# Optimization experiments

Measured on AMD Instinct MI355X. Metric: run time of the kernel, lower is better.

Reference implementation:

```python
import jax, jax.numpy as jnp
import numpy as np

E = 256
H = 512
LN_EPS = 1e-5
NORM_EPS = 1e-12


def setup_inputs() -> dict:
    key = jax.random.key(0)
    ks = jax.random.split(key, 8)
    B, N, M = 8, 128, 128
    track_features = jax.random.normal(ks[0], (B, N, E), dtype=jnp.float32)
    det_features = jax.random.normal(ks[1], (B, M, E), dtype=jnp.float32)
    # MLP params (torch Linear default init style: uniform, but values irrelevant for correctness harness)
    lim1 = 1.0 / np.sqrt(3 * E)
    W1 = jax.random.uniform(ks[2], (3 * E, H), minval=-lim1, maxval=lim1, dtype=jnp.float32)
    b1 = jax.random.uniform(ks[3], (H,), minval=-lim1, maxval=lim1, dtype=jnp.float32)
    gamma = jnp.ones((H,), dtype=jnp.float32)
    beta = jnp.zeros((H,), dtype=jnp.float32)
    lim2 = 1.0 / np.sqrt(H)
    W2 = jax.random.uniform(ks[4], (H, 1), minval=-lim2, maxval=lim2, dtype=jnp.float32)
    b2 = jax.random.uniform(ks[5], (1,), minval=-lim2, maxval=lim2, dtype=jnp.float32)
    return {"track_features": track_features, "det_features": det_features,
            "W1": W1, "b1": b1, "gamma": gamma, "beta": beta, "W2": W2, "b2": b2}


def _l2_normalize(x):
    # F.normalize(x, dim=-1): x / max(||x||_2, eps)
    n = jnp.sqrt(jnp.sum(x * x, axis=-1, keepdims=True))
    return x / jnp.maximum(n, NORM_EPS)


def reference(track_features, det_features, W1, b1, gamma, beta, W2, b2):
    t = _l2_normalize(track_features)   # (B, N, E)
    d = _l2_normalize(det_features)     # (B, M, E)
    tb = t[:, :, None, :]               # (B, N, 1, E)
    db = d[:, None, :, :]               # (B, 1, M, E)
    B, N, _ = t.shape
    M = d.shape[1]
    diff = jnp.abs(tb - db)                                  # (B, N, M, E)
    pair = jnp.concatenate([jnp.broadcast_to(tb, (B, N, M, E)),
                            jnp.broadcast_to(db, (B, N, M, E)),
                            diff], axis=-1)                  # (B, N, M, 3E)
    h = jnp.einsum('bnme,eh->bnmh', pair, W1) + b1           # (B, N, M, H)
    mu = jnp.mean(h, axis=-1, keepdims=True)
    var = jnp.mean((h - mu) ** 2, axis=-1, keepdims=True)
    h = (h - mu) * jax.lax.rsqrt(var + LN_EPS) * gamma + beta
    h = h * jax.nn.sigmoid(h)                                # SiLU
    out = jnp.einsum('bnmh,ho->bnmo', h, W2)[..., 0] + b2[0]  # (B, N, M)
    return out
```

## Files before the change

kernel.cpp:

```cpp
#include <hip/hip_runtime.h>
#include <hip/hip_bf16.h>
#include <cstdint>

typedef __bf16 bf16x8 __attribute__((ext_vector_type(8)));
typedef float f32x4 __attribute__((ext_vector_type(4)));

#define E_DIM 256
#define H_DIM 512
#define TSTR 260

__global__ __launch_bounds__(256)
void w1conv_kernel(const float* __restrict__ W1, __bf16* __restrict__ W1cc) {
    int u = blockIdx.x * 256 + threadIdx.x;
    int j   = u & 3;
    int h   = (u >> 2) & 511;
    int c   = (u >> 11) & 7;
    int mat = u >> 14;
    bf16x8 v;
#pragma unroll
    for (int i = 0; i < 8; ++i)
        v[i] = (__bf16)W1[(size_t)(mat * 256 + c * 32 + j * 8 + i) * H_DIM + h];
    *(bf16x8*)(W1cc + ((size_t)(mat * 8 + c) * 512 + h) * 32 + j * 8) = v;
}

__global__ __launch_bounds__(512, 4)
void pq_mfma_kernel(const float* __restrict__ track, const float* __restrict__ det,
                    const __bf16* __restrict__ W1cc, const float* __restrict__ b1,
                    float* __restrict__ P, float* __restrict__ Q) {
    __shared__ __align__(16) __bf16 Ash[32 * 256];
    __shared__ float sclS[32];

    int tid  = threadIdx.x;
    int lane = tid & 63;
    int wave = tid >> 6;
    int lq   = lane >> 4;
    int lc   = lane & 15;

    int blk  = blockIdx.x;
    int mat  = blk >> 6;
    int rowg = (blk >> 1) & 31;
    int half = blk & 1;
    int r0   = rowg * 32;
    int h0   = half * 256;
    const float* src = mat ? det : track;

#pragma unroll
    for (int i = 0; i < 4; ++i) {
        int row = wave * 4 + i;
        float4 x = ((const float4*)(src + (size_t)(r0 + row) * E_DIM))[lane];
        float ss = x.x*x.x + x.y*x.y + x.z*x.z + x.w*x.w;
#pragma unroll
        for (int off = 32; off > 0; off >>= 1) ss += __shfl_xor(ss, off);
        if (lane == 0) sclS[row] = 1.0f / fmaxf(sqrtf(ss), 1e-12f);
    }
    __syncthreads();

#pragma unroll
    for (int r = 0; r < 2; ++r) {
        int row = r * 16 + lc;
        float st = sclS[row];
        const float* gp = src + (size_t)(r0 + row) * E_DIM + wave * 32 + lq * 8;
        float4 t0 = *(const float4*)gp;
        float4 t1 = *(const float4*)(gp + 4);
        bf16x8 v;
        v[0] = (__bf16)(t0.x * st); v[1] = (__bf16)(t0.y * st);
        v[2] = (__bf16)(t0.z * st); v[3] = (__bf16)(t0.w * st);
        v[4] = (__bf16)(t1.x * st); v[5] = (__bf16)(t1.y * st);
        v[6] = (__bf16)(t1.z * st); v[7] = (__bf16)(t1.w * st);
        *(bf16x8*)&Ash[(size_t)(r * 512 + wave * 64 + lane) * 8] = v;
    }
    __syncthreads();

    const uint4* Wg = (const uint4*)W1cc + (mat ? 16384 : 0);
    int hb = h0 + wave * 32 + lc;
    bf16x8 bwA[2], bwB[2];
#pragma unroll
    for (int ht = 0; ht < 2; ++ht)
        bwA[ht] = __builtin_bit_cast(bf16x8, Wg[(hb + ht * 16) * 4 + lq]);

    f32x4 acc[2][2];
#pragma unroll
    for (int pt = 0; pt < 2; ++pt)
#pragma unroll
        for (int ht = 0; ht < 2; ++ht)
            acc[pt][ht] = (f32x4){0.f, 0.f, 0.f, 0.f};

#pragma unroll
    for (int c = 0; c < 8; ++c) {
        bf16x8* cur = (c & 1) ? bwB : bwA;
        bf16x8* nxt = (c & 1) ? bwA : bwB;
        if (c < 7) {
#pragma unroll
            for (int ht = 0; ht < 2; ++ht)
                nxt[ht] = __builtin_bit_cast(bf16x8, Wg[(c + 1) * 2048 + (hb + ht * 16) * 4 + lq]);
        }
#pragma unroll
        for (int pt = 0; pt < 2; ++pt) {
            bf16x8 af = *(const bf16x8*)&Ash[(size_t)((pt * 8 + c) * 64 + lane) * 8];
#pragma unroll
            for (int ht = 0; ht < 2; ++ht)
                acc[pt][ht] = __builtin_amdgcn_mfma_f32_16x16x32_bf16(cur[ht], af, acc[pt][ht], 0, 0, 0);
        }
    }

    float* dst = mat ? Q : P;
#pragma unroll
    for (int ht = 0; ht < 2; ++ht) {
        int h = h0 + wave * 32 + ht * 16 + lq * 4;
        f32x4 bvv = (f32x4){0.f, 0.f, 0.f, 0.f};
        if (!mat) bvv = *(const f32x4*)&b1[h];
#pragma unroll
        for (int pt = 0; pt < 2; ++pt) {
            f32x4 o = acc[pt][ht] + bvv;
            *(f32x4*)&dst[(size_t)(r0 + pt * 16 + lc) * H_DIM + h] = o;
        }
    }
}

__global__ __launch_bounds__(512, 4)
void main_kernel(const float* __restrict__ track, const float* __restrict__ det,
                 const __bf16* __restrict__ W1cc,
                 const float* __restrict__ P, const float* __restrict__ Q,
                 const float* __restrict__ gamma, const float* __restrict__ beta,
                 const float* __restrict__ W2, const float* __restrict__ b2,
                 float* __restrict__ out) {
    __shared__ __align__(16) char SMEM[49408];
    __bf16* Ash  = (__bf16*)SMEM;
    float*  tsl  = (float*)(SMEM + 32768);
    float*  dsl  = (float*)(SMEM + 41088);
    float*  LNr1 = (float*)(SMEM + 32768);
    float*  LNr2 = (float*)(SMEM + 35072);
    float*  Red2 = (float*)(SMEM + 37376);
    float*  MuS  = (float*)(SMEM + 39680);
    float*  RsS  = (float*)(SMEM + 39936);
    __shared__ float sclT[8], sclD[8];

    int tid  = threadIdx.x;
    int lane = tid & 63;
    int wave = tid >> 6;
    int lq   = lane >> 4;
    int lc   = lane & 15;

    int blk = blockIdx.x;
    int b   = blk >> 8;
    int n0  = ((blk >> 4) & 15) * 8;
    int m0  = (blk & 15) * 8;

    float4 tstage = ((const float4*)(track + (size_t)(b * 128 + n0 + wave) * E_DIM))[lane];
    float4 dstage = ((const float4*)(det   + (size_t)(b * 128 + m0 + wave) * E_DIM))[lane];

    const uint4* Wg = (const uint4*)W1cc + 32768;
    int hb = wave * 64 + lc;
    bf16x8 bwA[4], bwB[4];
#pragma unroll
    for (int ht = 0; ht < 4; ++ht)
        bwA[ht] = __builtin_bit_cast(bf16x8, Wg[(hb + ht * 16) * 4 + lq]);

    {
        float a = tstage.x*tstage.x + tstage.y*tstage.y + tstage.z*tstage.z + tstage.w*tstage.w;
        float d = dstage.x*dstage.x + dstage.y*dstage.y + dstage.z*dstage.z + dstage.w*dstage.w;
#pragma unroll
        for (int off = 32; off > 0; off >>= 1) { a += __shfl_xor(a, off); d += __shfl_xor(d, off); }
        if (lane == 0) {
            sclT[wave] = 1.0f / fmaxf(sqrtf(a), 1e-12f);
            sclD[wave] = 1.0f / fmaxf(sqrtf(d), 1e-12f);
        }
    }
    *(float4*)&tsl[wave * TSTR + lane * 4] = tstage;
    *(float4*)&dsl[wave * TSTR + lane * 4] = dstage;
    __syncthreads();

    {
        int k0 = wave * 32 + lq * 8;
        int ml = lane & 7;
        float sd = sclD[ml];
        const float* dr = dsl + ml * TSTR + k0;
        float4 d0 = *(const float4*)dr;
        float4 d1 = *(const float4*)(dr + 4);
#pragma unroll
        for (int r = 0; r < 4; ++r) {
            int nl = r * 2 + (lc >> 3);
            float st = sclT[nl];
            const float* tr = tsl + nl * TSTR + k0;
            float4 t0 = *(const float4*)tr;
            float4 t1 = *(const float4*)(tr + 4);
            bf16x8 v;
            v[0] = (__bf16)fabsf(t0.x * st - d0.x * sd);
            v[1] = (__bf16)fabsf(t0.y * st - d0.y * sd);
            v[2] = (__bf16)fabsf(t0.z * st - d0.z * sd);
            v[3] = (__bf16)fabsf(t0.w * st - d0.w * sd);
            v[4] = (__bf16)fabsf(t1.x * st - d1.x * sd);
            v[5] = (__bf16)fabsf(t1.y * st - d1.y * sd);
            v[6] = (__bf16)fabsf(t1.z * st - d1.z * sd);
            v[7] = (__bf16)fabsf(t1.w * st - d1.w * sd);
            *(bf16x8*)&Ash[(size_t)(r * 512 + wave * 64 + lane) * 8] = v;
        }
    }

    const float* Pb = P + (size_t)(b * 128 + n0) * H_DIM;
    const float* Qb = Q + (size_t)(b * 128 + m0) * H_DIM;
    f32x4 acc[4][4];
    {
        f32x4 qv[4];
#pragma unroll
        for (int ht = 0; ht < 4; ++ht)
            qv[ht] = *(const f32x4*)&Qb[(size_t)(lc & 7) * H_DIM + wave * 64 + ht * 16 + lq * 4];
#pragma unroll
        for (int pt = 0; pt < 4; ++pt) {
            int n = pt * 2 + (lc >> 3);
#pragma unroll
            for (int ht = 0; ht < 4; ++ht) {
                f32x4 pv = *(const f32x4*)&Pb[(size_t)n * H_DIM + wave * 64 + ht * 16 + lq * 4];
                acc[pt][ht] = pv + qv[ht];
            }
        }
    }
    __syncthreads();

#pragma unroll
    for (int c = 0; c < 8; ++c) {
        bf16x8* cur = (c & 1) ? bwB : bwA;
        bf16x8* nxt = (c & 1) ? bwA : bwB;
        if (c < 7) {
#pragma unroll
            for (int ht = 0; ht < 4; ++ht)
                nxt[ht] = __builtin_bit_cast(bf16x8, Wg[(c + 1) * 2048 + (hb + ht * 16) * 4 + lq]);
        }
#pragma unroll
        for (int pt = 0; pt < 4; ++pt) {
            bf16x8 af = *(const bf16x8*)&Ash[(size_t)((pt * 8 + c) * 64 + lane) * 8];
#pragma unroll
            for (int ht = 0; ht < 4; ++ht)
                acc[pt][ht] = __builtin_amdgcn_mfma_f32_16x16x32_bf16(cur[ht], af, acc[pt][ht], 0, 0, 0);
        }
    }

#pragma unroll
    for (int pt = 0; pt < 4; ++pt) {
        float s1 = 0.f, s2 = 0.f;
#pragma unroll
        for (int ht = 0; ht < 4; ++ht)
#pragma unroll
            for (int rg = 0; rg < 4; ++rg) {
                float v = acc[pt][ht][rg];
                s1 += v; s2 += v * v;
            }
        s1 += __shfl_xor(s1, 16); s2 += __shfl_xor(s2, 16);
        s1 += __shfl_xor(s1, 32); s2 += __shfl_xor(s2, 32);
        if (lq == 0) {
            LNr1[(pt * 16 + lc) * 9 + wave] = s1;
            LNr2[(pt * 16 + lc) * 9 + wave] = s2;
        }
    }
    __syncthreads();
    if (tid < 64) {
        float S1 = 0.f, S2 = 0.f;
#pragma unroll
        for (int w = 0; w < 8; ++w) { S1 += LNr1[tid * 9 + w]; S2 += LNr2[tid * 9 + w]; }
        float mu = S1 * (1.0f / 512.0f);
        float var = S2 * (1.0f / 512.0f) - mu * mu;
        MuS[tid] = mu;
        RsS[tid] = rsqrtf(var + 1e-5f);
    }
    __syncthreads();

    float mus[4], rss[4];
#pragma unroll
    for (int pt = 0; pt < 4; ++pt) { mus[pt] = MuS[pt * 16 + lc]; rss[pt] = RsS[pt * 16 + lc]; }
    float ca[4] = {0.f, 0.f, 0.f, 0.f};
#pragma unroll
    for (int ht = 0; ht < 4; ++ht) {
        int h = wave * 64 + ht * 16 + lq * 4;
        f32x4 g  = *(const f32x4*)&gamma[h];
        f32x4 bb = *(const f32x4*)&beta[h];
        f32x4 w  = *(const f32x4*)&W2[h];
#pragma unroll
        for (int pt = 0; pt < 4; ++pt) {
#pragma unroll
            for (int rg = 0; rg < 4; ++rg) {
                float x = (acc[pt][ht][rg] - mus[pt]) * rss[pt] * g[rg] + bb[rg];
                float sg = __builtin_amdgcn_rcpf(1.0f + __expf(-x));
                ca[pt] += x * sg * w[rg];
            }
        }
    }
#pragma unroll
    for (int pt = 0; pt < 4; ++pt) {
        float c = ca[pt];
        c += __shfl_xor(c, 16);
        c += __shfl_xor(c, 32);
        if (lq == 0) Red2[(pt * 16 + lc) * 9 + wave] = c;
    }
    __syncthreads();
    if (tid < 64) {
        float o = b2[0];
#pragma unroll
        for (int w = 0; w < 8; ++w) o += Red2[tid * 9 + w];
        int n = n0 + (tid >> 3);
        int m = m0 + (tid & 7);
        out[(size_t)(b * 128 + n) * 128 + m] = o;
    }
}

extern "C" void kernel_launch(void* const* d_in, const int* in_sizes, int n_in,
                              void* d_out, int out_size, void* d_ws, size_t ws_size,
                              hipStream_t stream) {
    const float* track = (const float*)d_in[0];
    const float* det   = (const float*)d_in[1];
    const float* W1    = (const float*)d_in[2];
    const float* b1    = (const float*)d_in[3];
    const float* gamma = (const float*)d_in[4];
    const float* beta  = (const float*)d_in[5];
    const float* W2    = (const float*)d_in[6];
    const float* b2    = (const float*)d_in[7];
    float* out = (float*)d_out;

    char* ws = (char*)d_ws;
    float*  P     = (float*)(ws);
    float*  Q     = (float*)(ws + (2u << 20));
    __bf16* W1cc  = (__bf16*)(ws + (4u << 20));

    w1conv_kernel<<<192, 256, 0, stream>>>(W1, W1cc);
    pq_mfma_kernel<<<128, 512, 0, stream>>>(track, det, W1cc, b1, P, Q);
    main_kernel<<<2048, 512, 0, stream>>>(track, det, W1cc, P, Q, gamma, beta, W2, b2, out);
}
```

Measured before the change: 157.1 us.

## Halve main kernel pair tile to 8x4 and triple-buffer W1 register prefetch

Each block of the main kernel now handles an 8x4 track-det tile instead of 8x8, so the grid doubles to 4096 blocks. The accumulator array halves and LDS shrinks, and the LN reduction buffers are aliased onto the A-tile region. The W1 fragment prefetch goes from two to three register buffers with a distance of two chunks. The aim is higher occupancy and better latency hiding. In exchange, every W1 fragment and every track/P row is loaded twice as often, since the reuse across the det dimension is halved.

```diff
diff --git a/kernel.cpp b/kernel.cpp
--- a/kernel.cpp
+++ b/kernel.cpp
@@ -124,16 +124,16 @@
                  const float* __restrict__ gamma, const float* __restrict__ beta,
                  const float* __restrict__ W2, const float* __restrict__ b2,
                  float* __restrict__ out) {
-    __shared__ __align__(16) char SMEM[49408];
+    __shared__ __align__(16) char SMEM[28864];
     __bf16* Ash  = (__bf16*)SMEM;
-    float*  tsl  = (float*)(SMEM + 32768);
-    float*  dsl  = (float*)(SMEM + 41088);
-    float*  LNr1 = (float*)(SMEM + 32768);
-    float*  LNr2 = (float*)(SMEM + 35072);
-    float*  Red2 = (float*)(SMEM + 37376);
-    float*  MuS  = (float*)(SMEM + 39680);
-    float*  RsS  = (float*)(SMEM + 39936);
-    __shared__ float sclT[8], sclD[8];
+    float*  tsl  = (float*)(SMEM + 16384);
+    float*  dsl  = (float*)(SMEM + 24704);
+    float*  LNr1 = (float*)SMEM;
+    float*  LNr2 = (float*)(SMEM + 1536);
+    float*  Red2 = (float*)(SMEM + 3072);
+    float*  MuS  = (float*)(SMEM + 4608);
+    float*  RsS  = (float*)(SMEM + 4736);
+    __shared__ float sclT[8], sclD[4];
 
     int tid  = threadIdx.x;
     int lane = tid & 63;
@@ -142,44 +142,50 @@
     int lc   = lane & 15;
 
     int blk = blockIdx.x;
-    int b   = blk >> 8;
-    int n0  = ((blk >> 4) & 15) * 8;
-    int m0  = (blk & 15) * 8;
+    int b   = blk >> 9;
+    int n0  = ((blk >> 5) & 15) * 8;
+    int m0  = (blk & 31) * 4;
 
     float4 tstage = ((const float4*)(track + (size_t)(b * 128 + n0 + wave) * E_DIM))[lane];
-    float4 dstage = ((const float4*)(det   + (size_t)(b * 128 + m0 + wave) * E_DIM))[lane];
+    float4 dstage;
+    if (wave < 4)
+        dstage = ((const float4*)(det + (size_t)(b * 128 + m0 + wave) * E_DIM))[lane];
 
     const uint4* Wg = (const uint4*)W1cc + 32768;
     int hb = wave * 64 + lc;
-    bf16x8 bwA[4], bwB[4];
-#pragma unroll
-    for (int ht = 0; ht < 4; ++ht)
-        bwA[ht] = __builtin_bit_cast(bf16x8, Wg[(hb + ht * 16) * 4 + lq]);
+    bf16x8 bw[3][4];
+#pragma unroll
+    for (int ht = 0; ht < 4; ++ht) {
+        bw[0][ht] = __builtin_bit_cast(bf16x8, Wg[(hb + ht * 16) * 4 + lq]);
+        bw[1][ht] = __builtin_bit_cast(bf16x8, Wg[2048 + (hb + ht * 16) * 4 + lq]);
+    }
 
     {
         float a = tstage.x*tstage.x + tstage.y*tstage.y + tstage.z*tstage.z + tstage.w*tstage.w;
+#pragma unroll
+        for (int off = 32; off > 0; off >>= 1) a += __shfl_xor(a, off);
+        if (lane == 0) sclT[wave] = 1.0f / fmaxf(sqrtf(a), 1e-12f);
+    }
+    *(float4*)&tsl[wave * TSTR + lane * 4] = tstage;
+    if (wave < 4) {
         float d = dstage.x*dstage.x + dstage.y*dstage.y + dstage.z*dstage.z + dstage.w*dstage.w;
 #pragma unroll
-        for (int off = 32; off > 0; off >>= 1) { a += __shfl_xor(a, off); d += __shfl_xor(d, off); }
-        if (lane == 0) {
-            sclT[wave] = 1.0f / fmaxf(sqrtf(a), 1e-12f);
-            sclD[wave] = 1.0f / fmaxf(sqrtf(d), 1e-12f);
-        }
-    }
-    *(float4*)&tsl[wave * TSTR + lane * 4] = tstage;
-    *(float4*)&dsl[wave * TSTR + lane * 4] = dstage;
+        for (int off = 32; off > 0; off >>= 1) d += __shfl_xor(d, off);
+        if (lane == 0) sclD[wave] = 1.0f / fmaxf(sqrtf(d), 1e-12f);
+        *(float4*)&dsl[wave * TSTR + lane * 4] = dstage;
+    }
     __syncthreads();
 
     {
         int k0 = wave * 32 + lq * 8;
-        int ml = lane & 7;
+        int ml = lc & 3;
         float sd = sclD[ml];
         const float* dr = dsl + ml * TSTR + k0;
         float4 d0 = *(const float4*)dr;
         float4 d1 = *(const float4*)(dr + 4);
 #pragma unroll
-        for (int r = 0; r < 4; ++r) {
-            int nl = r * 2 + (lc >> 3);
+        for (int rp = 0; rp < 2; ++rp) {
+            int nl = rp * 4 + (lc >> 2);
             float st = sclT[nl];
             const float* tr = tsl + nl * TSTR + k0;
             float4 t0 = *(const float4*)tr;
@@ -193,21 +199,21 @@
             v[5] = (__bf16)fabsf(t1.y * st - d1.y * sd);
             v[6] = (__bf16)fabsf(t1.z * st - d1.z * sd);
             v[7] = (__bf16)fabsf(t1.w * st - d1.w * sd);
-            *(bf16x8*)&Ash[(size_t)(r * 512 + wave * 64 + lane) * 8] = v;
+            *(bf16x8*)&Ash[(size_t)(rp * 512 + wave * 64 + lane) * 8] = v;
         }
     }
 
     const float* Pb = P + (size_t)(b * 128 + n0) * H_DIM;
     const float* Qb = Q + (size_t)(b * 128 + m0) * H_DIM;
-    f32x4 acc[4][4];
+    f32x4 acc[2][4];
     {
         f32x4 qv[4];
 #pragma unroll
         for (int ht = 0; ht < 4; ++ht)
-            qv[ht] = *(const f32x4*)&Qb[(size_t)(lc & 7) * H_DIM + wave * 64 + ht * 16 + lq * 4];
-#pragma unroll
-        for (int pt = 0; pt < 4; ++pt) {
-            int n = pt * 2 + (lc >> 3);
+            qv[ht] = *(const f32x4*)&Qb[(size_t)(lc & 3) * H_DIM + wave * 64 + ht * 16 + lq * 4];
+#pragma unroll
+        for (int pt = 0; pt < 2; ++pt) {
+            int n = pt * 4 + (lc >> 2);
 #pragma unroll
             for (int ht = 0; ht < 4; ++ht) {
                 f32x4 pv = *(const f32x4*)&Pb[(size_t)n * H_DIM + wave * 64 + ht * 16 + lq * 4];
@@ -219,24 +225,24 @@
 
 #pragma unroll
     for (int c = 0; c < 8; ++c) {
-        bf16x8* cur = (c & 1) ? bwB : bwA;
-        bf16x8* nxt = (c & 1) ? bwA : bwB;
-        if (c < 7) {
+        if (c < 6) {
+            int nb = (c + 2) % 3;
 #pragma unroll
             for (int ht = 0; ht < 4; ++ht)
-                nxt[ht] = __builtin_bit_cast(bf16x8, Wg[(c + 1) * 2048 + (hb + ht * 16) * 4 + lq]);
-        }
-#pragma unroll
-        for (int pt = 0; pt < 4; ++pt) {
+                bw[nb][ht] = __builtin_bit_cast(bf16x8, Wg[(c + 2) * 2048 + (hb + ht * 16) * 4 + lq]);
+        }
+        int cur = c % 3;
+#pragma unroll
+        for (int pt = 0; pt < 2; ++pt) {
             bf16x8 af = *(const bf16x8*)&Ash[(size_t)((pt * 8 + c) * 64 + lane) * 8];
 #pragma unroll
             for (int ht = 0; ht < 4; ++ht)
-                acc[pt][ht] = __builtin_amdgcn_mfma_f32_16x16x32_bf16(cur[ht], af, acc[pt][ht], 0, 0, 0);
-        }
-    }
-
-#pragma unroll
-    for (int pt = 0; pt < 4; ++pt) {
+                acc[pt][ht] = __builtin_amdgcn_mfma_f32_16x16x32_bf16(bw[cur][ht], af, acc[pt][ht], 0, 0, 0);
+        }
+    }
+
+#pragma unroll
+    for (int pt = 0; pt < 2; ++pt) {
         float s1 = 0.f, s2 = 0.f;
 #pragma unroll
         for (int ht = 0; ht < 4; ++ht)
@@ -253,7 +259,7 @@
         }
     }
     __syncthreads();
-    if (tid < 64) {
+    if (tid < 32) {
         float S1 = 0.f, S2 = 0.f;
 #pragma unroll
         for (int w = 0; w < 8; ++w) { S1 += LNr1[tid * 9 + w]; S2 += LNr2[tid * 9 + w]; }
@@ -264,10 +270,10 @@
     }
     __syncthreads();
 
-    float mus[4], rss[4];
-#pragma unroll
-    for (int pt = 0; pt < 4; ++pt) { mus[pt] = MuS[pt * 16 + lc]; rss[pt] = RsS[pt * 16 + lc]; }
-    float ca[4] = {0.f, 0.f, 0.f, 0.f};
+    float mus[2], rss[2];
+#pragma unroll
+    for (int pt = 0; pt < 2; ++pt) { mus[pt] = MuS[pt * 16 + lc]; rss[pt] = RsS[pt * 16 + lc]; }
+    float ca[2] = {0.f, 0.f};
 #pragma unroll
     for (int ht = 0; ht < 4; ++ht) {
         int h = wave * 64 + ht * 16 + lq * 4;
@@ -275,7 +281,7 @@
         f32x4 bb = *(const f32x4*)&beta[h];
         f32x4 w  = *(const f32x4*)&W2[h];
 #pragma unroll
-        for (int pt = 0; pt < 4; ++pt) {
+        for (int pt = 0; pt < 2; ++pt) {
 #pragma unroll
             for (int rg = 0; rg < 4; ++rg) {
                 float x = (acc[pt][ht][rg] - mus[pt]) * rss[pt] * g[rg] + bb[rg];
@@ -285,19 +291,19 @@
         }
     }
 #pragma unroll
-    for (int pt = 0; pt < 4; ++pt) {
+    for (int pt = 0; pt < 2; ++pt) {
         float c = ca[pt];
         c += __shfl_xor(c, 16);
         c += __shfl_xor(c, 32);
         if (lq == 0) Red2[(pt * 16 + lc) * 9 + wave] = c;
     }
     __syncthreads();
-    if (tid < 64) {
+    if (tid < 32) {
         float o = b2[0];
 #pragma unroll
         for (int w = 0; w < 8; ++w) o += Red2[tid * 9 + w];
-        int n = n0 + (tid >> 3);
-        int m = m0 + (tid & 7);
+        int n = n0 + (tid >> 2);
+        int m = m0 + (tid & 3);
         out[(size_t)(b * 128 + n) * 128 + m] = o;
     }
 }
@@ -322,5 +328,5 @@
 
     w1conv_kernel<<<192, 256, 0, stream>>>(W1, W1cc);
     pq_mfma_kernel<<<128, 512, 0, stream>>>(track, det, W1cc, b1, P, Q);
-    main_kernel<<<2048, 512, 0, stream>>>(track, det, W1cc, P, Q, gamma, beta, W2, b2, out);
+    main_kernel<<<4096, 512, 0, stream>>>(track, det, W1cc, P, Q, gamma, beta, W2, b2, out);
 }
```

After: 181.0 us. 15.2% more time.
